# Kernel tuning notes

Measured on AMD Instinct MI355X. Metric: run time of the kernel, lower is better.

Reference implementation:

```python
import jax, jax.numpy as jnp
import numpy as np

N = 50000      # nodes
E = 800000     # edges (avg degree 16)
D_IN = 64      # input feature dim
HID = 128      # hidden dim
NEG = 0.2      # LeakyReLU slope (PyG GATConv default)
EPS = 1e-5     # BatchNorm eps


def _bn(x, g, b):
    mu = jnp.mean(x, 0)
    var = jnp.var(x, 0)
    return (x - mu) * jax.lax.rsqrt(var + EPS) * g + b


def _gat(x, src, dst, W, a_s, a_d, bias, heads, out_c, concat):
    # PyG GATConv: h = xW per head, e_ij = LeakyReLU(a_s.h_i + a_d.h_j),
    # softmax over incoming edges of each dst node, weighted scatter-sum.
    n = x.shape[0]
    h = (x @ W).reshape(n, heads, out_c)                 # [N,H,C]
    sc_s = jnp.sum(h * a_s, -1)                          # [N,H]
    sc_d = jnp.sum(h * a_d, -1)                          # [N,H]
    e = jax.nn.leaky_relu(sc_s[src] + sc_d[dst], NEG)    # [E,H]
    m = jax.lax.stop_gradient(jax.ops.segment_max(e, dst, num_segments=n))
    e = jnp.exp(e - m[dst])
    s = jax.ops.segment_sum(e, dst, num_segments=n)
    alpha = e / (s[dst] + 1e-16)                         # [E,H]
    out = jax.ops.segment_sum(h[src] * alpha[:, :, None], dst, num_segments=n)
    out = out.reshape(n, heads * out_c) if concat else out.mean(1)
    return out + bias


def setup_inputs() -> dict:
    ks = jax.random.split(jax.random.key(0), 20)
    r = lambda i, sh, s=0.05: jax.random.normal(ks[i], sh, jnp.float32) * s
    return dict(
        x=jax.random.normal(ks[0], (N, D_IN), jnp.float32),
        edge_index=jax.random.randint(ks[1], (2, E), 0, N, dtype=jnp.int32),
        in_gamma=jnp.ones((D_IN,)), in_beta=jnp.zeros((D_IN,)),
        proj_W=r(2, (D_IN, HID)), proj_b=jnp.zeros((HID,)),
        skip_W=r(3, (HID, HID)), skip_b=jnp.zeros((HID,)),
        conv1_W=r(4, (HID, HID)), conv1_as=r(5, (4, 32)), conv1_ad=r(6, (4, 32)), conv1_b=jnp.zeros((HID,)),
        bn1_g=jnp.ones((HID,)), bn1_b=jnp.zeros((HID,)),
        conv2_W=r(7, (HID, HID)), conv2_as=r(8, (4, 32)), conv2_ad=r(9, (4, 32)), conv2_b=jnp.zeros((HID,)),
        bn2_g=jnp.ones((HID,)), bn2_b=jnp.zeros((HID,)),
        conv3_W=r(10, (HID, HID)), conv3_as=r(11, (1, HID)), conv3_ad=r(12, (1, HID)), conv3_b=jnp.zeros((HID,)),
        bn3_g=jnp.ones((HID,)), bn3_b=jnp.zeros((HID,)),
        cls_W1=r(13, (HID, 64)), cls_b1=jnp.zeros((64,)),
        cls_W2=r(14, (64, 32)), cls_b2=jnp.zeros((32,)),
        cls_W3=r(15, (32, 2)), cls_b3=jnp.zeros((2,)),
        conf_W=r(16, (HID, 1)), conf_b=jnp.zeros((1,)),
    )


def reference(x, edge_index, in_gamma, in_beta, proj_W, proj_b, skip_W, skip_b,
              conv1_W, conv1_as, conv1_ad, conv1_b, bn1_g, bn1_b,
              conv2_W, conv2_as, conv2_ad, conv2_b, bn2_g, bn2_b,
              conv3_W, conv3_as, conv3_ad, conv3_b, bn3_g, bn3_b,
              cls_W1, cls_b1, cls_W2, cls_b2, cls_W3, cls_b3, conf_W, conf_b):
    n = x.shape[0]
    # PyG GATConv add_self_loops=True
    loop = jnp.arange(n, dtype=edge_index.dtype)
    src = jnp.concatenate([edge_index[0], loop])
    dst = jnp.concatenate([edge_index[1], loop])

    h = _bn(x, in_gamma, in_beta)
    h = h @ proj_W + proj_b
    hr = jax.nn.relu(h)
    h_skip = hr @ skip_W + skip_b

    h = _gat(hr, src, dst, conv1_W, conv1_as, conv1_ad, conv1_b, 4, 32, True)
    h = jax.nn.relu(_bn(h, bn1_g, bn1_b))
    h = _gat(h, src, dst, conv2_W, conv2_as, conv2_ad, conv2_b, 4, 32, True)
    h = jax.nn.relu(_bn(h, bn2_g, bn2_b))
    h = _gat(h, src, dst, conv3_W, conv3_as, conv3_ad, conv3_b, 1, HID, False)
    h = jax.nn.relu(_bn(h, bn3_g, bn3_b) + h_skip)

    c = jax.nn.relu(h @ cls_W1 + cls_b1)
    c = jax.nn.relu(c @ cls_W2 + cls_b2)
    logits = c @ cls_W3 + cls_b3
    conf = jax.nn.sigmoid(h @ conf_W + conf_b)
    return logits, conf
```

## Files before the change

### kernel.cpp

```cpp
#include <hip/hip_runtime.h>
#include <cstdint>
#include <cstddef>

#define NN 50000
#define EE 800000
#define TOT_E (NN + EE)
#define NBK 391
#define BCAP 2560

typedef __attribute__((ext_vector_type(8))) short short8;
typedef __attribute__((ext_vector_type(4))) float f32x4;

static __device__ __forceinline__ unsigned short f2bf(float f) {
  union { float f; unsigned u; } v;
  v.f = f;
  unsigned r = v.u + 0x7FFFu + ((v.u >> 16) & 1u);
  return (unsigned short)(r >> 16);
}
static __device__ __forceinline__ float bf2f(unsigned short u) {
  union { unsigned u; float f; } v;
  v.u = ((unsigned)u) << 16;
  return v.f;
}
static __device__ __forceinline__ float bf2f_lo(unsigned u) {
  union { unsigned u; float f; } v;
  v.u = u << 16;
  return v.f;
}
static __device__ __forceinline__ float bf2f_hi(unsigned u) {
  union { unsigned u; float f; } v;
  v.u = u & 0xFFFF0000u;
  return v.f;
}

__global__ __launch_bounds__(512) void k_bin(const int* __restrict__ ei,
                                             int* __restrict__ gpos,
                                             unsigned* __restrict__ binned) {
  __shared__ int cnt[512];
  __shared__ int base[512];
  int tx = threadIdx.x;
  cnt[tx] = 0;
  __syncthreads();
  int e0 = blockIdx.x * 3125;
  int e1 = e0 + 3125;
  if (e1 > EE) e1 = EE;
  for (int i = e0 + tx; i < e1; i += 512) {
    int d = ei[EE + i];
    atomicAdd(&cnt[d >> 7], 1);
  }
  __syncthreads();
  if (tx < NBK) {
    int c = cnt[tx];
    base[tx] = c ? atomicAdd(&gpos[tx], c) : 0;
    cnt[tx] = 0;
  }
  __syncthreads();
  for (int i = e0 + tx; i < e1; i += 512) {
    int s = ei[i];
    int d = ei[EE + i];
    int b = d >> 7;
    int slot = base[b] + atomicAdd(&cnt[b], 1);
    if (slot < BCAP) binned[(size_t)b * BCAP + slot] = (unsigned)s | ((unsigned)(d & 127) << 16);
  }
}
__global__ __launch_bounds__(512) void k_bscan(const int* __restrict__ gpos,
                                               int* __restrict__ ebase,
                                               int* __restrict__ rowp) {
  __shared__ int sh[512];
  int tx = threadIdx.x;
  int v = 0;
  if (tx < NBK) {
    int nodes = NN - (tx << 7);
    if (nodes > 128) nodes = 128;
    int g = gpos[tx];
    if (g > BCAP) g = BCAP;
    v = g + nodes;
  }
  sh[tx] = v;
  __syncthreads();
  for (int off = 1; off < 512; off <<= 1) {
    int t = (tx >= off) ? sh[tx - off] : 0;
    __syncthreads();
    sh[tx] += t;
    __syncthreads();
  }
  if (tx < NBK) ebase[tx] = sh[tx] - v;
  if (tx == NBK - 1) rowp[NN] = sh[tx];
}
__global__ __launch_bounds__(256) void k_bucket(const unsigned* __restrict__ binned,
                                                const int* __restrict__ gpos,
                                                const int* __restrict__ ebase,
                                                int* __restrict__ rowp,
                                                int* __restrict__ srcl) {
  __shared__ int cnt[128], offs[128], cur[128];
  int b = blockIdx.x, tid = threadIdx.x;
  int n0 = b << 7;
  int nodes = NN - n0;
  if (nodes > 128) nodes = 128;
  int ne = gpos[b];
  if (ne > BCAP) ne = BCAP;
  int eb = ebase[b];
  if (tid < 128) cnt[tid] = (tid < nodes) ? 1 : 0;
  __syncthreads();
  const unsigned* bb = binned + (size_t)b * BCAP;
  for (int i = tid; i < ne; i += 256) atomicAdd(&cnt[bb[i] >> 16], 1);
  __syncthreads();
  if (tid < 128) offs[tid] = cnt[tid];
  __syncthreads();
  for (int o = 1; o < 128; o <<= 1) {
    int t = (tid < 128 && tid >= o) ? offs[tid - o] : 0;
    __syncthreads();
    if (tid < 128) offs[tid] += t;
    __syncthreads();
  }
  if (tid < 128 && tid < nodes) {
    int ex = offs[tid] - cnt[tid];
    rowp[n0 + tid] = eb + ex;
    srcl[eb + ex] = n0 + tid;
    cur[tid] = ex + 1;
  }
  __syncthreads();
  for (int i = tid; i < ne; i += 256) {
    unsigned e = bb[i];
    int r = atomicAdd(&cur[e >> 16], 1);
    srcl[eb + r] = (int)(e & 0xFFFFu);
  }
}

__global__ __launch_bounds__(256) void k_bn_stats64(const float* __restrict__ x,
                                                    float* __restrict__ sums) {
  int col = threadIdx.x & 63;
  int rsub = threadIdx.x >> 6;
  float s = 0.f, q = 0.f;
  for (int r = blockIdx.x * 4 + rsub; r < NN; r += gridDim.x * 4) {
    float v = x[(size_t)r * 64 + col];
    s += v;
    q += v * v;
  }
  __shared__ float bs[256], bq[256];
  bs[threadIdx.x] = s;
  bq[threadIdx.x] = q;
  __syncthreads();
  if (threadIdx.x < 64) {
#pragma unroll
    for (int i = 1; i < 4; ++i) {
      s += bs[threadIdx.x + i * 64];
      q += bq[threadIdx.x + i * 64];
    }
    atomicAdd(&sums[col], s);
    atomicAdd(&sums[64 + col], q);
  }
}

__global__ void k_reorder_all(const float* __restrict__ projW, const float* __restrict__ skipW,
                              const float* __restrict__ c1W, const float* __restrict__ c2W,
                              const float* __restrict__ c3W, const float* __restrict__ W1,
                              const float* __restrict__ cw, unsigned short* __restrict__ wr) {
  int o = blockIdx.x * 256 + threadIdx.x;
  if (o < 8192) {
    int off = o;
    int j = off & 7, t = off >> 3;
    int q = t & 3; t >>= 2;
    int c = t & 15; t >>= 4;
    int kb = t & 1, ct = t >> 1;
    int k = kb * 32 + q * 8 + j, col = ct * 16 + c;
    wr[o] = f2bf(projW[(size_t)k * 128 + col]);
  } else if (o < 73728) {
    int region = (o - 8192) >> 14;
    int off = (o - 8192) & 16383;
    const float* W = region == 0 ? skipW : region == 1 ? c1W : region == 2 ? c2W : c3W;
    int j = off & 7, t = off >> 3;
    int q = t & 3; t >>= 2;
    int c = t & 15; t >>= 4;
    int kb = t & 3, ct = t >> 2;
    int k = kb * 32 + q * 8 + j, col = ct * 16 + c;
    wr[o] = f2bf(W[(size_t)k * 128 + col]);
  } else if (o < 83968) {
    int off = o - 73728;
    int j = off & 7, t = off >> 3;
    int q = t & 3; t >>= 2;
    int c = t & 15; t >>= 4;
    int kb = t & 3, ct = t >> 2;
    int k = kb * 32 + q * 8 + j, col = ct * 16 + c;
    float v = 0.f;
    if (col < 64) v = W1[(size_t)k * 64 + col];
    else if (col == 64) v = cw[k];
    wr[o] = f2bf(v);
  }
}

template <int NH, int NT, int F>
static __device__ __forceinline__ void write_scores(const f32x4 (&acc)[F][NT],
                                                    const float* __restrict__ a_s,
                                                    const float* __restrict__ a_d,
                                                    int r0, int lane, int wv,
                                                    float* __restrict__ scs,
                                                    float* __restrict__ scd) {
  const int lr = lane & 15, lg = lane >> 4;
  float asv[NT], adv[NT];
#pragma unroll
  for (int ct = 0; ct < NT; ++ct) {
    asv[ct] = a_s[ct * 16 + lr];
    adv[ct] = a_d[ct * 16 + lr];
  }
  float ps[F][4][NH], pd[F][4][NH];
#pragma unroll
  for (int f = 0; f < F; ++f)
#pragma unroll
    for (int r = 0; r < 4; ++r)
#pragma unroll
      for (int h = 0; h < NH; ++h) { ps[f][r][h] = 0.f; pd[f][r][h] = 0.f; }
#pragma unroll
  for (int f = 0; f < F; ++f)
#pragma unroll
    for (int ct = 0; ct < NT; ++ct) {
      int h = (NH == 1) ? 0 : (ct >> 1);
#pragma unroll
      for (int r = 0; r < 4; ++r) {
        ps[f][r][h] = fmaf(acc[f][ct][r], asv[ct], ps[f][r][h]);
        pd[f][r][h] = fmaf(acc[f][ct][r], adv[ct], pd[f][r][h]);
      }
    }
#pragma unroll
  for (int off = 1; off < 16; off <<= 1)
#pragma unroll
    for (int f = 0; f < F; ++f)
#pragma unroll
      for (int r = 0; r < 4; ++r)
#pragma unroll
        for (int h = 0; h < NH; ++h) {
          ps[f][r][h] += __shfl_xor(ps[f][r][h], off);
          pd[f][r][h] += __shfl_xor(pd[f][r][h], off);
        }
  if (lr == 0) {
#pragma unroll
    for (int f = 0; f < F; ++f) {
      int rowb = r0 + (wv * F + f) * 16 + lg * 4;
#pragma unroll
      for (int r = 0; r < 4; ++r) {
        int gr = rowb + r;
        if (gr < NN) {
          if (NH == 4) {
            float4 vs = make_float4(ps[f][r][0], ps[f][r][1], ps[f][r][2], ps[f][r][3]);
            float4 vd = make_float4(pd[f][r][0], pd[f][r][1], pd[f][r][2], pd[f][r][3]);
            *(float4*)(scs + (size_t)gr * 4) = vs;
            *(float4*)(scd + (size_t)gr * 4) = vd;
          } else {
            scs[gr] = ps[f][r][0];
            scd[gr] = pd[f][r][0];
          }
        }
      }
    }
  }
}

template <int BIAS, int RELU, int NT, int F>
static __device__ __forceinline__ void write_out_bf(const f32x4 (&acc)[F][NT],
                                                    const float* __restrict__ bias,
                                                    int r0, int lane, int wv,
                                                    unsigned short* __restrict__ out) {
  const int lr = lane & 15, lg = lane >> 4;
#pragma unroll
  for (int f = 0; f < F; ++f) {
    int rowb = r0 + (wv * F + f) * 16 + lg * 4;
#pragma unroll
    for (int ct = 0; ct < NT; ++ct) {
      int col = ct * 16 + lr;
      float bb = BIAS ? bias[col] : 0.f;
#pragma unroll
      for (int r = 0; r < 4; ++r) {
        int gr = rowb + r;
        if (gr < NN) {
          float o = acc[f][ct][r] + bb;
          if (RELU) o = fmaxf(o, 0.f);
          out[(size_t)gr * 128 + col] = f2bf(o);
        }
      }
    }
  }
}

template <int BM, int K, int NT, int ABF, int BN, int BNP, int BIAS, int RELU, int OUTM, int SCH>
__global__ __launch_bounds__(256) void k_mgemm(
    const void* __restrict__ Ain, const unsigned short* __restrict__ Bw,
    const float* __restrict__ bias,
    const float* __restrict__ bnsums, const float* __restrict__ bng,
    const float* __restrict__ bnb,
    const unsigned short* __restrict__ skip,
    const float* __restrict__ a_s, const float* __restrict__ a_d,
    const float* __restrict__ confb,
    void* __restrict__ Cout, float* __restrict__ conf,
    float* __restrict__ scs, float* __restrict__ scd,
    const float* __restrict__ W2, const float* __restrict__ b2,
    const float* __restrict__ W3, const float* __restrict__ b3,
    float* __restrict__ logits) {
  constexpr int KB = K / 32;
  constexpr int RT = BM / 16;
  constexpr int F = BM / 64;
  __shared__ __align__(16) unsigned short sm[(RT + NT) * KB * 512];
  __shared__ float bnsc[128], bnsh[128];
  const int tid = threadIdx.x;
  const int r0 = blockIdx.x * BM;

  if constexpr (BN) {
    if (tid < K) {
      float s, q;
      if constexpr (BNP) {
        s = 0.f; q = 0.f;
#pragma unroll 8
        for (int pp = 0; pp < 64; ++pp) {
          s += bnsums[pp * 256 + tid];
          q += bnsums[pp * 256 + 128 + tid];
        }
      } else {
        s = bnsums[tid];
        q = bnsums[K + tid];
      }
      float invM = 1.f / (float)NN;
      float mu = s * invM;
      float var = q * invM - mu * mu;
      float sc = bng[tid] * rsqrtf(var + 1e-5f);
      bnsc[tid] = sc;
      bnsh[tid] = bnb[tid] - mu * sc;
    }
    __syncthreads();
  }

  if constexpr (ABF) {
    const unsigned short* A = (const unsigned short*)Ain;
    constexpr int IT = BM * (K / 8) / 256;
#pragma unroll
    for (int it = 0; it < IT; ++it) {
      int idx = it * 256 + tid;
      int r = idx / (K / 8);
      int k = (idx % (K / 8)) * 8;
      int gr = r0 + r;
      union { uint4 u4; unsigned short us[8]; } v;
      v.u4 = make_uint4(0, 0, 0, 0);
      if (gr < NN) v.u4 = *(const uint4*)(A + (size_t)gr * K + k);
      if constexpr (BN) {
        union { uint4 u4; unsigned short us[8]; } sv;
        if (BN == 3) {
          sv.u4 = make_uint4(0, 0, 0, 0);
          if (gr < NN) sv.u4 = *(const uint4*)(skip + (size_t)gr * 128 + k);
        }
#pragma unroll
        for (int j = 0; j < 8; ++j) {
          float f = bf2f(v.us[j]) * bnsc[k + j] + bnsh[k + j];
          if (BN == 3) f += bf2f(sv.us[j]);
          if (BN >= 2) f = fmaxf(f, 0.f);
          v.us[j] = f2bf(f);
        }
      }
      *(uint4*)&sm[((r >> 4) * KB + (k >> 5)) * 512 + (r & 15) * 32 + (k & 31)] = v.u4;
    }
  } else {
    const float* A = (const float*)Ain;
    constexpr int IT = BM * (K / 4) / 256;
#pragma unroll
    for (int it = 0; it < IT; ++it) {
      int idx = it * 256 + tid;
      int r = idx / (K / 4);
      int k = (idx % (K / 4)) * 4;
      int gr = r0 + r;
      float4 av = make_float4(0.f, 0.f, 0.f, 0.f);
      if (gr < NN) av = *(const float4*)(A + (size_t)gr * K + k);
      if constexpr (BN) {
        av.x = av.x * bnsc[k + 0] + bnsh[k + 0];
        av.y = av.y * bnsc[k + 1] + bnsh[k + 1];
        av.z = av.z * bnsc[k + 2] + bnsh[k + 2];
        av.w = av.w * bnsc[k + 3] + bnsh[k + 3];
        if (BN >= 2) {
          av.x = fmaxf(av.x, 0.f); av.y = fmaxf(av.y, 0.f);
          av.z = fmaxf(av.z, 0.f); av.w = fmaxf(av.w, 0.f);
        }
      }
      ushort4 o;
      o.x = f2bf(av.x); o.y = f2bf(av.y); o.z = f2bf(av.z); o.w = f2bf(av.w);
      *(ushort4*)&sm[((r >> 4) * KB + (k >> 5)) * 512 + (r & 15) * 32 + (k & 31)] = o;
    }
  }
  {
    constexpr int BW = NT * KB * 512;
#pragma unroll
    for (int it = 0; it < BW / 2048; ++it) {
      int idx = it * 256 + tid;
      *(uint4*)&sm[RT * KB * 512 + idx * 8] = *(const uint4*)(Bw + idx * 8);
    }
  }
  __syncthreads();

  const int lane = tid & 63, wv = tid >> 6;
  const int lr = lane & 15, lg = lane >> 4;
  const int fidx = lr * 32 + lg * 8;
  f32x4 acc[F][NT];
#pragma unroll
  for (int f = 0; f < F; ++f)
#pragma unroll
    for (int ct = 0; ct < NT; ++ct) acc[f][ct] = (f32x4){0.f, 0.f, 0.f, 0.f};
#pragma unroll
  for (int kb = 0; kb < KB; ++kb) {
    short8 afr[F];
#pragma unroll
    for (int f = 0; f < F; ++f)
      afr[f] = *(const short8*)&sm[((wv * F + f) * KB + kb) * 512 + fidx];
#pragma unroll
    for (int ct = 0; ct < NT; ++ct) {
      short8 b = *(const short8*)&sm[((RT + ct) * KB + kb) * 512 + fidx];
#pragma unroll
      for (int f = 0; f < F; ++f)
        acc[f][ct] = __builtin_amdgcn_mfma_f32_16x16x32_bf16(afr[f], b, acc[f][ct], 0, 0, 0);
    }
  }

  if constexpr (SCH > 0) {
    write_scores<(SCH == 1) ? 1 : 4>(acc, a_s, a_d, r0, lane, wv, scs, scd);
  }

  if constexpr (OUTM == 2) {
    __syncthreads();
    unsigned short* c1s = sm;
    float* W2s = (float*)(sm + 8320);
    float* c2s = (float*)(sm + 12416);
    float* W3s = (float*)(sm + 20864);
    float* b2s = (float*)(sm + 20992);
    float* b3s = (float*)(sm + 21056);
    for (int i = tid; i < 2048; i += 256) W2s[i] = W2[i];
    if (tid < 64) W3s[tid] = W3[tid];
    if (tid < 32) b2s[tid] = b2[tid];
    if (tid < 2) b3s[tid] = b3[tid];
#pragma unroll
    for (int f = 0; f < F; ++f) {
      int lrow = (wv * F + f) * 16 + lg * 4;
#pragma unroll
      for (int ct = 0; ct < NT; ++ct) {
        int col = ct * 16 + lr;
        if (col < 64) {
          float bb = bias[col];
#pragma unroll
          for (int r = 0; r < 4; ++r)
            c1s[(lrow + r) * 65 + col] = f2bf(fmaxf(acc[f][ct][r] + bb, 0.f));
        } else if (col == 64) {
          float cb = confb[0];
#pragma unroll
          for (int r = 0; r < 4; ++r) {
            int gr = r0 + lrow + r;
            if (gr < NN) conf[gr] = 1.f / (1.f + __expf(-(acc[f][ct][r] + cb)));
          }
        }
      }
    }
    __syncthreads();
    {
      int node = tid & 127;
      int cb = (tid >> 7) * 16;
      float a2[16];
#pragma unroll
      for (int i = 0; i < 16; ++i) a2[i] = b2s[cb + i];
      for (int k = 0; k < 64; ++k) {
        float v = bf2f(c1s[node * 65 + k]);
#pragma unroll
        for (int i = 0; i < 16; ++i) a2[i] = fmaf(v, W2s[k * 32 + cb + i], a2[i]);
      }
#pragma unroll
      for (int i = 0; i < 16; ++i) c2s[node * 33 + cb + i] = fmaxf(a2[i], 0.f);
    }
    __syncthreads();
    {
      int node = tid >> 1, j = tid & 1;
      float s3 = b3s[j];
#pragma unroll 8
      for (int k = 0; k < 32; ++k) s3 = fmaf(c2s[node * 33 + k], W3s[k * 2 + j], s3);
      int gr = r0 + node;
      if (gr < NN) logits[(size_t)gr * 2 + j] = s3;
    }
  } else {
    write_out_bf<BIAS, RELU>(acc, bias, r0, lane, wv, (unsigned short*)Cout);
  }
}

__global__ __launch_bounds__(256) void k_mgemm_dual(
    const unsigned short* __restrict__ A, const unsigned short* __restrict__ Bw1,
    const float* __restrict__ bias1, const unsigned short* __restrict__ Bw2,
    const float* __restrict__ a_s, const float* __restrict__ a_d,
    unsigned short* __restrict__ Out1, unsigned short* __restrict__ Out2,
    float* __restrict__ scs, float* __restrict__ scd) {
  constexpr int KB = 4;
  __shared__ __align__(16) unsigned short sm[16 * KB * 512];
  const int tid = threadIdx.x;
  const int r0 = blockIdx.x * 128;
#pragma unroll
  for (int it = 0; it < 8; ++it) {
    int idx = it * 256 + tid;
    int r = idx >> 4;
    int k = (idx & 15) * 8;
    int gr = r0 + r;
    uint4 v = make_uint4(0, 0, 0, 0);
    if (gr < NN) v = *(const uint4*)(A + (size_t)gr * 128 + k);
    *(uint4*)&sm[((r >> 4) * KB + (k >> 5)) * 512 + (r & 15) * 32 + (k & 31)] = v;
  }
#pragma unroll
  for (int it = 0; it < 8; ++it) {
    int idx = it * 256 + tid;
    *(uint4*)&sm[8 * KB * 512 + idx * 8] = *(const uint4*)(Bw1 + idx * 8);
  }
  __syncthreads();
  const int lane = tid & 63, wv = tid >> 6;
  const int lr = lane & 15, lg = lane >> 4;
  const int fidx = lr * 32 + lg * 8;
  f32x4 acc[2][8];
#pragma unroll
  for (int f = 0; f < 2; ++f)
#pragma unroll
    for (int ct = 0; ct < 8; ++ct) acc[f][ct] = (f32x4){0.f, 0.f, 0.f, 0.f};
#pragma unroll
  for (int kb = 0; kb < KB; ++kb) {
    short8 a0 = *(const short8*)&sm[((wv * 2 + 0) * KB + kb) * 512 + fidx];
    short8 a1 = *(const short8*)&sm[((wv * 2 + 1) * KB + kb) * 512 + fidx];
#pragma unroll
    for (int ct = 0; ct < 8; ++ct) {
      short8 b = *(const short8*)&sm[((8 + ct) * KB + kb) * 512 + fidx];
      acc[0][ct] = __builtin_amdgcn_mfma_f32_16x16x32_bf16(a0, b, acc[0][ct], 0, 0, 0);
      acc[1][ct] = __builtin_amdgcn_mfma_f32_16x16x32_bf16(a1, b, acc[1][ct], 0, 0, 0);
    }
  }
  write_out_bf<1, 0>(acc, bias1, r0, lane, wv, Out1);
  __syncthreads();
#pragma unroll
  for (int it = 0; it < 8; ++it) {
    int idx = it * 256 + tid;
    *(uint4*)&sm[8 * KB * 512 + idx * 8] = *(const uint4*)(Bw2 + idx * 8);
  }
  __syncthreads();
#pragma unroll
  for (int f = 0; f < 2; ++f)
#pragma unroll
    for (int ct = 0; ct < 8; ++ct) acc[f][ct] = (f32x4){0.f, 0.f, 0.f, 0.f};
#pragma unroll
  for (int kb = 0; kb < KB; ++kb) {
    short8 a0 = *(const short8*)&sm[((wv * 2 + 0) * KB + kb) * 512 + fidx];
    short8 a1 = *(const short8*)&sm[((wv * 2 + 1) * KB + kb) * 512 + fidx];
#pragma unroll
    for (int ct = 0; ct < 8; ++ct) {
      short8 b = *(const short8*)&sm[((8 + ct) * KB + kb) * 512 + fidx];
      acc[0][ct] = __builtin_amdgcn_mfma_f32_16x16x32_bf16(a0, b, acc[0][ct], 0, 0, 0);
      acc[1][ct] = __builtin_amdgcn_mfma_f32_16x16x32_bf16(a1, b, acc[1][ct], 0, 0, 0);
    }
  }
  write_scores<4>(acc, a_s, a_d, r0, lane, wv, scs, scd);
  write_out_bf<0, 0>(acc, nullptr, r0, lane, wv, Out2);
}

template <int H>
__global__ __launch_bounds__(256) void k_agg(const unsigned short* __restrict__ hp,
                                             const float* __restrict__ scs,
                                             const float* __restrict__ scd,
                                             const int* __restrict__ rowp,
                                             const int* __restrict__ srcl,
                                             const float* __restrict__ bias,
                                             unsigned short* __restrict__ out,
                                             float* __restrict__ part) {
  __shared__ float ssum[8][144], ssq[8][144];
  int tid = threadIdx.x;
  int lane = tid & 63, wv = tid >> 6;
  int half = lane >> 5;
  int l32 = lane & 31;
  int g = l32 >> 4;
  int l16 = lane & 15;
  int n = (blockIdx.x * 4 + wv) * 2 + half;
  int c0 = l16 * 8;
  int hid = (H == 1) ? 0 : (l16 >> 2);
  float sd = scd[(size_t)n * H + hid];
  int beg = rowp[n], end = rowp[n + 1];
  int last = end - 1;
  float a[8];
#pragma unroll
  for (int i = 0; i < 8; ++i) a[i] = 0.f;
  float sw = 0.f;
  for (int k0 = beg + g * 4; k0 < end; k0 += 8) {
    int k1 = k0 + 1, k2 = k0 + 2, k3 = k0 + 3;
    int s0 = srcl[k0];
    int s1 = srcl[k1 <= last ? k1 : last];
    int s2 = srcl[k2 <= last ? k2 : last];
    int s3 = srcl[k3 <= last ? k3 : last];
    float e0 = scs[(size_t)s0 * H + hid] + sd;
    float e1 = scs[(size_t)s1 * H + hid] + sd;
    float e2 = scs[(size_t)s2 * H + hid] + sd;
    float e3 = scs[(size_t)s3 * H + hid] + sd;
    uint4 u0 = *(const uint4*)(hp + (size_t)s0 * 128 + c0);
    uint4 u1 = *(const uint4*)(hp + (size_t)s1 * 128 + c0);
    uint4 u2 = *(const uint4*)(hp + (size_t)s2 * 128 + c0);
    uint4 u3 = *(const uint4*)(hp + (size_t)s3 * 128 + c0);
    e0 = fmaxf(e0, 0.f) + 0.2f * fminf(e0, 0.f);
    e1 = fmaxf(e1, 0.f) + 0.2f * fminf(e1, 0.f);
    e2 = fmaxf(e2, 0.f) + 0.2f * fminf(e2, 0.f);
    e3 = fmaxf(e3, 0.f) + 0.2f * fminf(e3, 0.f);
    float w0 = __expf(e0);
    float w1 = (k1 <= last) ? __expf(e1) : 0.f;
    float w2 = (k2 <= last) ? __expf(e2) : 0.f;
    float w3 = (k3 <= last) ? __expf(e3) : 0.f;
    a[0] = fmaf(w0, bf2f_lo(u0.x), a[0]); a[1] = fmaf(w0, bf2f_hi(u0.x), a[1]);
    a[2] = fmaf(w0, bf2f_lo(u0.y), a[2]); a[3] = fmaf(w0, bf2f_hi(u0.y), a[3]);
    a[4] = fmaf(w0, bf2f_lo(u0.z), a[4]); a[5] = fmaf(w0, bf2f_hi(u0.z), a[5]);
    a[6] = fmaf(w0, bf2f_lo(u0.w), a[6]); a[7] = fmaf(w0, bf2f_hi(u0.w), a[7]);
    a[0] = fmaf(w1, bf2f_lo(u1.x), a[0]); a[1] = fmaf(w1, bf2f_hi(u1.x), a[1]);
    a[2] = fmaf(w1, bf2f_lo(u1.y), a[2]); a[3] = fmaf(w1, bf2f_hi(u1.y), a[3]);
    a[4] = fmaf(w1, bf2f_lo(u1.z), a[4]); a[5] = fmaf(w1, bf2f_hi(u1.z), a[5]);
    a[6] = fmaf(w1, bf2f_lo(u1.w), a[6]); a[7] = fmaf(w1, bf2f_hi(u1.w), a[7]);
    a[0] = fmaf(w2, bf2f_lo(u2.x), a[0]); a[1] = fmaf(w2, bf2f_hi(u2.x), a[1]);
    a[2] = fmaf(w2, bf2f_lo(u2.y), a[2]); a[3] = fmaf(w2, bf2f_hi(u2.y), a[3]);
    a[4] = fmaf(w2, bf2f_lo(u2.z), a[4]); a[5] = fmaf(w2, bf2f_hi(u2.z), a[5]);
    a[6] = fmaf(w2, bf2f_lo(u2.w), a[6]); a[7] = fmaf(w2, bf2f_hi(u2.w), a[7]);
    a[0] = fmaf(w3, bf2f_lo(u3.x), a[0]); a[1] = fmaf(w3, bf2f_hi(u3.x), a[1]);
    a[2] = fmaf(w3, bf2f_lo(u3.y), a[2]); a[3] = fmaf(w3, bf2f_hi(u3.y), a[3]);
    a[4] = fmaf(w3, bf2f_lo(u3.z), a[4]); a[5] = fmaf(w3, bf2f_hi(u3.z), a[5]);
    a[6] = fmaf(w3, bf2f_lo(u3.w), a[6]); a[7] = fmaf(w3, bf2f_hi(u3.w), a[7]);
    sw += (w0 + w1) + (w2 + w3);
  }
#pragma unroll
  for (int i = 0; i < 8; ++i) a[i] += __shfl_xor(a[i], 16);
  sw += __shfl_xor(sw, 16);
  int slice = wv * 2 + half;
  if (g == 0) {
    float inv = 1.f / (sw + 1e-16f);
    unsigned wb[4];
    int ib = c0 + l16;
#pragma unroll
    for (int j = 0; j < 4; ++j) {
      float o0 = a[2 * j] * inv + bias[c0 + 2 * j];
      float o1 = a[2 * j + 1] * inv + bias[c0 + 2 * j + 1];
      ssum[slice][ib + 2 * j] = o0;
      ssum[slice][ib + 2 * j + 1] = o1;
      ssq[slice][ib + 2 * j] = o0 * o0;
      ssq[slice][ib + 2 * j + 1] = o1 * o1;
      wb[j] = (unsigned)f2bf(o0) | ((unsigned)f2bf(o1) << 16);
    }
    *(uint4*)(out + (size_t)n * 128 + c0) = make_uint4(wb[0], wb[1], wb[2], wb[3]);
  }
  __syncthreads();
  if (tid < 128) {
    int idx = tid + (tid >> 3);
    float s = 0.f, q = 0.f;
#pragma unroll
    for (int sl = 0; sl < 8; ++sl) {
      s += ssum[sl][idx];
      q += ssq[sl][idx];
    }
    int pb = (blockIdx.x & 63) * 256;
    atomicAdd(&part[pb + tid], s);
    atomicAdd(&part[pb + 128 + tid], q);
  }
}

extern "C" void kernel_launch(void* const* d_in, const int* in_sizes, int n_in,
                              void* d_out, int out_size, void* d_ws, size_t ws_size,
                              hipStream_t stream) {
  (void)in_sizes; (void)n_in; (void)out_size; (void)ws_size;
  const float* x       = (const float*)d_in[0];
  const int*   ei      = (const int*)d_in[1];
  const float* in_g    = (const float*)d_in[2];
  const float* in_b    = (const float*)d_in[3];
  const float* projW   = (const float*)d_in[4];
  const float* projb   = (const float*)d_in[5];
  const float* skipW   = (const float*)d_in[6];
  const float* skipb   = (const float*)d_in[7];
  const float* c1W     = (const float*)d_in[8];
  const float* c1as    = (const float*)d_in[9];
  const float* c1ad    = (const float*)d_in[10];
  const float* c1b     = (const float*)d_in[11];
  const float* bn1g    = (const float*)d_in[12];
  const float* bn1b    = (const float*)d_in[13];
  const float* c2W     = (const float*)d_in[14];
  const float* c2as    = (const float*)d_in[15];
  const float* c2ad    = (const float*)d_in[16];
  const float* c2b     = (const float*)d_in[17];
  const float* bn2g    = (const float*)d_in[18];
  const float* bn2b    = (const float*)d_in[19];
  const float* c3W     = (const float*)d_in[20];
  const float* c3as    = (const float*)d_in[21];
  const float* c3ad    = (const float*)d_in[22];
  const float* c3b     = (const float*)d_in[23];
  const float* bn3g    = (const float*)d_in[24];
  const float* bn3b    = (const float*)d_in[25];
  const float* clsW1   = (const float*)d_in[26];
  const float* clsb1   = (const float*)d_in[27];
  const float* clsW2   = (const float*)d_in[28];
  const float* clsb2   = (const float*)d_in[29];
  const float* clsW3   = (const float*)d_in[30];
  const float* clsb3   = (const float*)d_in[31];
  const float* confW   = (const float*)d_in[32];
  const float* confb   = (const float*)d_in[33];

  float* out_logits = (float*)d_out;
  float* out_conf   = (float*)d_out + (size_t)NN * 2;

  char* p = (char*)d_ws;
  auto alloc = [&](size_t bytes) -> char* {
    char* r = p;
    p += (bytes + 255) & ~(size_t)255;
    return r;
  };
  unsigned short* hr  = (unsigned short*)alloc((size_t)NN * 128 * 2);
  unsigned short* hsk = (unsigned short*)alloc((size_t)NN * 128 * 2);
  unsigned short* hb  = (unsigned short*)alloc((size_t)NN * 128 * 2);
  unsigned short* agA = (unsigned short*)alloc((size_t)NN * 128 * 2);
  unsigned short* agB = (unsigned short*)alloc((size_t)NN * 128 * 2);
  float* scs   = (float*)alloc((size_t)NN * 4 * 4);
  float* scd   = (float*)alloc((size_t)NN * 4 * 4);
  char*  zr    = alloc(2048 + 1024 + 3 * 65536);
  int*   gpos  = (int*)zr;
  float* stats = (float*)(zr + 2048);
  float* part1 = stats + 256;
  float* part2 = part1 + 16384;
  float* part3 = part2 + 16384;
  int*   rowp  = (int*)alloc((size_t)(NN + 1) * 4);
  int*   ebase = (int*)alloc((size_t)NBK * 4);
  unsigned* binned = (unsigned*)alloc((size_t)NBK * BCAP * 4);
  int*   srcl  = (int*)alloc((size_t)TOT_E * 4);
  unsigned short* wr = (unsigned short*)alloc(83968 * 2);
  unsigned short* wr_proj = wr;
  unsigned short* wr_skip = wr + 8192;
  unsigned short* wr_c1   = wr + 24576;
  unsigned short* wr_c2   = wr + 40960;
  unsigned short* wr_c3   = wr + 57344;
  unsigned short* wr_cls  = wr + 73728;

  const int GB64  = (NN + 63) / 64;
  const int GB128 = (NN + 127) / 128;
  const int AB    = NN / 8;

  k_reorder_all<<<328, 256, 0, stream>>>(projW, skipW, c1W, c2W, c3W, clsW1, confW, wr);
  hipMemsetAsync(zr, 0, 2048 + 1024 + 3 * 65536, stream);

  k_bin<<<256, 512, 0, stream>>>(ei, gpos, binned);
  k_bscan<<<1, 512, 0, stream>>>(gpos, ebase, rowp);
  k_bucket<<<NBK, 256, 0, stream>>>(binned, gpos, ebase, rowp, srcl);

  k_bn_stats64<<<256, 256, 0, stream>>>(x, stats);

  k_mgemm<64, 64, 8, 0, 1, 0, 1, 1, 1, 0><<<GB64, 256, 0, stream>>>(
      x, wr_proj, projb, stats, in_g, in_b, nullptr, nullptr, nullptr, nullptr,
      hr, nullptr, nullptr, nullptr, nullptr, nullptr, nullptr, nullptr, nullptr);

  k_mgemm_dual<<<GB128, 256, 0, stream>>>(hr, wr_skip, skipb, wr_c1, c1as, c1ad,
                                          hsk, hb, scs, scd);
  k_agg<4><<<AB, 256, 0, stream>>>(hb, scs, scd, rowp, srcl, c1b, agA, part1);

  k_mgemm<64, 128, 8, 1, 2, 1, 0, 0, 1, 4><<<GB64, 256, 0, stream>>>(
      agA, wr_c2, nullptr, part1, bn1g, bn1b, nullptr, c2as, c2ad, nullptr,
      hb, nullptr, scs, scd, nullptr, nullptr, nullptr, nullptr, nullptr);
  k_agg<4><<<AB, 256, 0, stream>>>(hb, scs, scd, rowp, srcl, c2b, agB, part2);

  k_mgemm<64, 128, 8, 1, 2, 1, 0, 0, 1, 1><<<GB64, 256, 0, stream>>>(
      agB, wr_c3, nullptr, part2, bn2g, bn2b, nullptr, c3as, c3ad, nullptr,
      hb, nullptr, scs, scd, nullptr, nullptr, nullptr, nullptr, nullptr);
  k_agg<1><<<AB, 256, 0, stream>>>(hb, scs, scd, rowp, srcl, c3b, agA, part3);

  k_mgemm<128, 128, 5, 1, 3, 1, 1, 0, 2, 0><<<GB128, 256, 0, stream>>>(
      agA, wr_cls, clsb1, part3, bn3g, bn3b, hsk, nullptr, nullptr, confb,
      nullptr, out_conf, nullptr, nullptr, clsW2, clsb2, clsW3, clsb3, out_logits);
}
```

Baseline: 250.5 us.

## Merge weight reorder, input BN stats and edge binning into one prep kernel

Folds the weight reordering, input BatchNorm statistics and edge binning into a single heterogeneous launch that dispatches on block index. The per-bucket prefix scan moves into the bucket kernel as a redundant per-block reduction, which removes the separate single-block scan kernel. The input BN stats are now written as per-block partials instead of atomics, and the aggregation partial buffers shrink from 64 to 32 slots. The aggregation loop also prefetches the next source indices one iteration ahead, so the gather latency can overlap with compute. Together these cut kernel launches and serial dependencies, at the cost of extra redundant work in every bucket block.

After: 246.5 us. Within noise of the previous version (-1.6%).

```diff
diff --git a/kernel.cpp b/kernel.cpp
--- a/kernel.cpp
+++ b/kernel.cpp
@@ -33,73 +33,133 @@
   return v.f;
 }
 
-__global__ __launch_bounds__(512) void k_bin(const int* __restrict__ ei,
-                                             int* __restrict__ gpos,
-                                             unsigned* __restrict__ binned) {
-  __shared__ int cnt[512];
-  __shared__ int base[512];
+__global__ __launch_bounds__(512) void k_prep(
+    const float* __restrict__ projW, const float* __restrict__ skipW,
+    const float* __restrict__ c1W, const float* __restrict__ c2W,
+    const float* __restrict__ c3W, const float* __restrict__ W1,
+    const float* __restrict__ cw, unsigned short* __restrict__ wr,
+    const float* __restrict__ x, float* __restrict__ xpart,
+    const int* __restrict__ ei, int* __restrict__ gpos,
+    unsigned* __restrict__ binned) {
+  __shared__ float smf[1024];
   int tx = threadIdx.x;
-  cnt[tx] = 0;
-  __syncthreads();
-  int e0 = blockIdx.x * 3125;
-  int e1 = e0 + 3125;
-  if (e1 > EE) e1 = EE;
-  for (int i = e0 + tx; i < e1; i += 512) {
-    int d = ei[EE + i];
-    atomicAdd(&cnt[d >> 7], 1);
-  }
-  __syncthreads();
-  if (tx < NBK) {
-    int c = cnt[tx];
-    base[tx] = c ? atomicAdd(&gpos[tx], c) : 0;
+  int b = blockIdx.x;
+  if (b < 164) {
+    int o = b * 512 + tx;
+    if (o < 8192) {
+      int off = o;
+      int j = off & 7, t = off >> 3;
+      int q = t & 3; t >>= 2;
+      int c = t & 15; t >>= 4;
+      int kb = t & 1, ct = t >> 1;
+      int k = kb * 32 + q * 8 + j, col = ct * 16 + c;
+      wr[o] = f2bf(projW[(size_t)k * 128 + col]);
+    } else if (o < 73728) {
+      int region = (o - 8192) >> 14;
+      int off = (o - 8192) & 16383;
+      const float* W = region == 0 ? skipW : region == 1 ? c1W : region == 2 ? c2W : c3W;
+      int j = off & 7, t = off >> 3;
+      int q = t & 3; t >>= 2;
+      int c = t & 15; t >>= 4;
+      int kb = t & 3, ct = t >> 2;
+      int k = kb * 32 + q * 8 + j, col = ct * 16 + c;
+      wr[o] = f2bf(W[(size_t)k * 128 + col]);
+    } else if (o < 83968) {
+      int off = o - 73728;
+      int j = off & 7, t = off >> 3;
+      int q = t & 3; t >>= 2;
+      int c = t & 15; t >>= 4;
+      int kb = t & 3, ct = t >> 2;
+      int k = kb * 32 + q * 8 + j, col = ct * 16 + c;
+      float v = 0.f;
+      if (col < 64) v = W1[(size_t)k * 64 + col];
+      else if (col == 64) v = cw[k];
+      wr[o] = f2bf(v);
+    }
+  } else if (b < 228) {
+    int bi = b - 164;
+    int col = tx & 63;
+    int rsub = tx >> 6;
+    float s = 0.f, q = 0.f;
+    for (int r = bi * 8 + rsub; r < NN; r += 64 * 8) {
+      float v = x[(size_t)r * 64 + col];
+      s += v;
+      q += v * v;
+    }
+    smf[tx] = s;
+    smf[512 + tx] = q;
+    __syncthreads();
+    if (tx < 64) {
+#pragma unroll
+      for (int i = 1; i < 8; ++i) {
+        s += smf[tx + i * 64];
+        q += smf[512 + tx + i * 64];
+      }
+      xpart[bi * 128 + tx] = s;
+      xpart[bi * 128 + 64 + tx] = q;
+    }
+  } else {
+    int* cnt = (int*)smf;
+    int* base = (int*)smf + 512;
     cnt[tx] = 0;
-  }
-  __syncthreads();
-  for (int i = e0 + tx; i < e1; i += 512) {
-    int s = ei[i];
-    int d = ei[EE + i];
-    int b = d >> 7;
-    int slot = base[b] + atomicAdd(&cnt[b], 1);
-    if (slot < BCAP) binned[(size_t)b * BCAP + slot] = (unsigned)s | ((unsigned)(d & 127) << 16);
-  }
-}
-__global__ __launch_bounds__(512) void k_bscan(const int* __restrict__ gpos,
-                                               int* __restrict__ ebase,
-                                               int* __restrict__ rowp) {
-  __shared__ int sh[512];
-  int tx = threadIdx.x;
-  int v = 0;
-  if (tx < NBK) {
-    int nodes = NN - (tx << 7);
-    if (nodes > 128) nodes = 128;
-    int g = gpos[tx];
-    if (g > BCAP) g = BCAP;
-    v = g + nodes;
-  }
-  sh[tx] = v;
-  __syncthreads();
-  for (int off = 1; off < 512; off <<= 1) {
-    int t = (tx >= off) ? sh[tx - off] : 0;
-    __syncthreads();
-    sh[tx] += t;
-    __syncthreads();
-  }
-  if (tx < NBK) ebase[tx] = sh[tx] - v;
-  if (tx == NBK - 1) rowp[NN] = sh[tx];
-}
+    __syncthreads();
+    int e0 = (b - 228) * 3125;
+    int e1 = e0 + 3125;
+    if (e1 > EE) e1 = EE;
+    for (int i = e0 + tx; i < e1; i += 512) {
+      int d = ei[EE + i];
+      atomicAdd(&cnt[d >> 7], 1);
+    }
+    __syncthreads();
+    if (tx < NBK) {
+      int c = cnt[tx];
+      base[tx] = c ? atomicAdd(&gpos[tx], c) : 0;
+      cnt[tx] = 0;
+    }
+    __syncthreads();
+    for (int i = e0 + tx; i < e1; i += 512) {
+      int s = ei[i];
+      int d = ei[EE + i];
+      int bk = d >> 7;
+      int slot = base[bk] + atomicAdd(&cnt[bk], 1);
+      if (slot < BCAP)
+        binned[(size_t)bk * BCAP + slot] = (unsigned)s | ((unsigned)(d & 127) << 16);
+    }
+  }
+}
+
 __global__ __launch_bounds__(256) void k_bucket(const unsigned* __restrict__ binned,
                                                 const int* __restrict__ gpos,
-                                                const int* __restrict__ ebase,
                                                 int* __restrict__ rowp,
                                                 int* __restrict__ srcl) {
   __shared__ int cnt[128], offs[128], cur[128];
+  __shared__ int red[256], red2[256];
   int b = blockIdx.x, tid = threadIdx.x;
+  int accp = 0, acct = 0;
+  for (int i = tid; i < NBK; i += 256) {
+    int gv = gpos[i];
+    if (gv > BCAP) gv = BCAP;
+    if (i < b) accp += gv;
+    acct += gv;
+  }
+  red[tid] = accp;
+  red2[tid] = acct;
+  __syncthreads();
+  for (int o = 128; o; o >>= 1) {
+    if (tid < o) {
+      red[tid] += red[tid + o];
+      red2[tid] += red2[tid + o];
+    }
+    __syncthreads();
+  }
+  int eb = (b << 7) + red[0];
+  if (b == NBK - 1 && tid == 0) rowp[NN] = red2[0] + NN;
+
   int n0 = b << 7;
   int nodes = NN - n0;
   if (nodes > 128) nodes = 128;
   int ne = gpos[b];
   if (ne > BCAP) ne = BCAP;
-  int eb = ebase[b];
   if (tid < 128) cnt[tid] = (tid < nodes) ? 1 : 0;
   __syncthreads();
   const unsigned* bb = binned + (size_t)b * BCAP;
@@ -124,68 +184,6 @@
     unsigned e = bb[i];
     int r = atomicAdd(&cur[e >> 16], 1);
     srcl[eb + r] = (int)(e & 0xFFFFu);
-  }
-}
-
-__global__ __launch_bounds__(256) void k_bn_stats64(const float* __restrict__ x,
-                                                    float* __restrict__ sums) {
-  int col = threadIdx.x & 63;
-  int rsub = threadIdx.x >> 6;
-  float s = 0.f, q = 0.f;
-  for (int r = blockIdx.x * 4 + rsub; r < NN; r += gridDim.x * 4) {
-    float v = x[(size_t)r * 64 + col];
-    s += v;
-    q += v * v;
-  }
-  __shared__ float bs[256], bq[256];
-  bs[threadIdx.x] = s;
-  bq[threadIdx.x] = q;
-  __syncthreads();
-  if (threadIdx.x < 64) {
-#pragma unroll
-    for (int i = 1; i < 4; ++i) {
-      s += bs[threadIdx.x + i * 64];
-      q += bq[threadIdx.x + i * 64];
-    }
-    atomicAdd(&sums[col], s);
-    atomicAdd(&sums[64 + col], q);
-  }
-}
-
-__global__ void k_reorder_all(const float* __restrict__ projW, const float* __restrict__ skipW,
-                              const float* __restrict__ c1W, const float* __restrict__ c2W,
-                              const float* __restrict__ c3W, const float* __restrict__ W1,
-                              const float* __restrict__ cw, unsigned short* __restrict__ wr) {
-  int o = blockIdx.x * 256 + threadIdx.x;
-  if (o < 8192) {
-    int off = o;
-    int j = off & 7, t = off >> 3;
-    int q = t & 3; t >>= 2;
-    int c = t & 15; t >>= 4;
-    int kb = t & 1, ct = t >> 1;
-    int k = kb * 32 + q * 8 + j, col = ct * 16 + c;
-    wr[o] = f2bf(projW[(size_t)k * 128 + col]);
-  } else if (o < 73728) {
-    int region = (o - 8192) >> 14;
-    int off = (o - 8192) & 16383;
-    const float* W = region == 0 ? skipW : region == 1 ? c1W : region == 2 ? c2W : c3W;
-    int j = off & 7, t = off >> 3;
-    int q = t & 3; t >>= 2;
-    int c = t & 15; t >>= 4;
-    int kb = t & 3, ct = t >> 2;
-    int k = kb * 32 + q * 8 + j, col = ct * 16 + c;
-    wr[o] = f2bf(W[(size_t)k * 128 + col]);
-  } else if (o < 83968) {
-    int off = o - 73728;
-    int j = off & 7, t = off >> 3;
-    int q = t & 3; t >>= 2;
-    int c = t & 15; t >>= 4;
-    int kb = t & 3, ct = t >> 2;
-    int k = kb * 32 + q * 8 + j, col = ct * 16 + c;
-    float v = 0.f;
-    if (col < 64) v = W1[(size_t)k * 64 + col];
-    else if (col == 64) v = cw[k];
-    wr[o] = f2bf(v);
   }
 }
 
@@ -306,12 +304,19 @@
   if constexpr (BN) {
     if (tid < K) {
       float s, q;
-      if constexpr (BNP) {
+      if constexpr (BNP == 1) {
+        s = 0.f; q = 0.f;
+#pragma unroll 8
+        for (int pp = 0; pp < 32; ++pp) {
+          s += bnsums[pp * 256 + tid];
+          q += bnsums[pp * 256 + 128 + tid];
+        }
+      } else if constexpr (BNP == 2) {
         s = 0.f; q = 0.f;
 #pragma unroll 8
         for (int pp = 0; pp < 64; ++pp) {
-          s += bnsums[pp * 256 + tid];
-          q += bnsums[pp * 256 + 128 + tid];
+          s += bnsums[pp * 128 + tid];
+          q += bnsums[pp * 128 + 64 + tid];
         }
       } else {
         s = bnsums[tid];
@@ -578,12 +583,17 @@
 #pragma unroll
   for (int i = 0; i < 8; ++i) a[i] = 0.f;
   float sw = 0.f;
-  for (int k0 = beg + g * 4; k0 < end; k0 += 8) {
-    int k1 = k0 + 1, k2 = k0 + 2, k3 = k0 + 3;
-    int s0 = srcl[k0];
-    int s1 = srcl[k1 <= last ? k1 : last];
-    int s2 = srcl[k2 <= last ? k2 : last];
-    int s3 = srcl[k3 <= last ? k3 : last];
+  int k0 = beg + g * 4;
+  int s0 = srcl[(k0 + 0) <= last ? (k0 + 0) : last];
+  int s1 = srcl[(k0 + 1) <= last ? (k0 + 1) : last];
+  int s2 = srcl[(k0 + 2) <= last ? (k0 + 2) : last];
+  int s3 = srcl[(k0 + 3) <= last ? (k0 + 3) : last];
+  for (; k0 < end; k0 += 8) {
+    int np = k0 + 8;
+    int t0 = srcl[(np + 0) <= last ? (np + 0) : last];
+    int t1 = srcl[(np + 1) <= last ? (np + 1) : last];
+    int t2 = srcl[(np + 2) <= last ? (np + 2) : last];
+    int t3 = srcl[(np + 3) <= last ? (np + 3) : last];
     float e0 = scs[(size_t)s0 * H + hid] + sd;
     float e1 = scs[(size_t)s1 * H + hid] + sd;
     float e2 = scs[(size_t)s2 * H + hid] + sd;
@@ -597,9 +607,9 @@
     e2 = fmaxf(e2, 0.f) + 0.2f * fminf(e2, 0.f);
     e3 = fmaxf(e3, 0.f) + 0.2f * fminf(e3, 0.f);
     float w0 = __expf(e0);
-    float w1 = (k1 <= last) ? __expf(e1) : 0.f;
-    float w2 = (k2 <= last) ? __expf(e2) : 0.f;
-    float w3 = (k3 <= last) ? __expf(e3) : 0.f;
+    float w1 = (k0 + 1 <= last) ? __expf(e1) : 0.f;
+    float w2 = (k0 + 2 <= last) ? __expf(e2) : 0.f;
+    float w3 = (k0 + 3 <= last) ? __expf(e3) : 0.f;
     a[0] = fmaf(w0, bf2f_lo(u0.x), a[0]); a[1] = fmaf(w0, bf2f_hi(u0.x), a[1]);
     a[2] = fmaf(w0, bf2f_lo(u0.y), a[2]); a[3] = fmaf(w0, bf2f_hi(u0.y), a[3]);
     a[4] = fmaf(w0, bf2f_lo(u0.z), a[4]); a[5] = fmaf(w0, bf2f_hi(u0.z), a[5]);
@@ -617,6 +627,7 @@
     a[4] = fmaf(w3, bf2f_lo(u3.z), a[4]); a[5] = fmaf(w3, bf2f_hi(u3.z), a[5]);
     a[6] = fmaf(w3, bf2f_lo(u3.w), a[6]); a[7] = fmaf(w3, bf2f_hi(u3.w), a[7]);
     sw += (w0 + w1) + (w2 + w3);
+    s0 = t0; s1 = t1; s2 = t2; s3 = t3;
   }
 #pragma unroll
   for (int i = 0; i < 8; ++i) a[i] += __shfl_xor(a[i], 16);
@@ -647,7 +658,7 @@
       s += ssum[sl][idx];
       q += ssq[sl][idx];
     }
-    int pb = (blockIdx.x & 63) * 256;
+    int pb = (blockIdx.x & 31) * 256;
     atomicAdd(&part[pb + tid], s);
     atomicAdd(&part[pb + 128 + tid], q);
   }
@@ -708,14 +719,13 @@
   unsigned short* agB = (unsigned short*)alloc((size_t)NN * 128 * 2);
   float* scs   = (float*)alloc((size_t)NN * 4 * 4);
   float* scd   = (float*)alloc((size_t)NN * 4 * 4);
-  char*  zr    = alloc(2048 + 1024 + 3 * 65536);
+  char*  zr    = alloc(2048 + 3 * 32768);
   int*   gpos  = (int*)zr;
-  float* stats = (float*)(zr + 2048);
-  float* part1 = stats + 256;
-  float* part2 = part1 + 16384;
-  float* part3 = part2 + 16384;
+  float* part1 = (float*)(zr + 2048);
+  float* part2 = part1 + 8192;
+  float* part3 = part2 + 8192;
+  float* xpart = (float*)alloc(64 * 128 * 4);
   int*   rowp  = (int*)alloc((size_t)(NN + 1) * 4);
-  int*   ebase = (int*)alloc((size_t)NBK * 4);
   unsigned* binned = (unsigned*)alloc((size_t)NBK * BCAP * 4);
   int*   srcl  = (int*)alloc((size_t)TOT_E * 4);
   unsigned short* wr = (unsigned short*)alloc(83968 * 2);
@@ -730,17 +740,14 @@
   const int GB128 = (NN + 127) / 128;
   const int AB    = NN / 8;
 
-  k_reorder_all<<<328, 256, 0, stream>>>(projW, skipW, c1W, c2W, c3W, clsW1, confW, wr);
-  hipMemsetAsync(zr, 0, 2048 + 1024 + 3 * 65536, stream);
-
-  k_bin<<<256, 512, 0, stream>>>(ei, gpos, binned);
-  k_bscan<<<1, 512, 0, stream>>>(gpos, ebase, rowp);
-  k_bucket<<<NBK, 256, 0, stream>>>(binned, gpos, ebase, rowp, srcl);
-
-  k_bn_stats64<<<256, 256, 0, stream>>>(x, stats);
-
-  k_mgemm<64, 64, 8, 0, 1, 0, 1, 1, 1, 0><<<GB64, 256, 0, stream>>>(
-      x, wr_proj, projb, stats, in_g, in_b, nullptr, nullptr, nullptr, nullptr,
+  hipMemsetAsync(zr, 0, 2048 + 3 * 32768, stream);
+
+  k_prep<<<484, 512, 0, stream>>>(projW, skipW, c1W, c2W, c3W, clsW1, confW, wr,
+                                  x, xpart, ei, gpos, binned);
+  k_bucket<<<NBK, 256, 0, stream>>>(binned, gpos, rowp, srcl);
+
+  k_mgemm<64, 64, 8, 0, 1, 2, 1, 1, 1, 0><<<GB64, 256, 0, stream>>>(
+      x, wr_proj, projb, xpart, in_g, in_b, nullptr, nullptr, nullptr, nullptr,
       hr, nullptr, nullptr, nullptr, nullptr, nullptr, nullptr, nullptr, nullptr);
 
   k_mgemm_dual<<<GB128, 256, 0, stream>>>(hr, wr_skip, skipb, wr_c1, c1as, c1ad,
```
